# Kernel tuning notes

Hardware: AMD Instinct MI355X
Metric: run time of the kernel (lower is better)

Reference implementation:

```python
import jax, jax.numpy as jnp
import numpy as np
from jax import lax

H = 12  # num_heads (from init_kwargs)


def _orthogonal_landmarks(q, num_landmarks):
    # q: (B, N, D) already scaled. Faithful to torch loop: recursively pick the
    # point whose max |cos sim| to the already-selected landmarks is minimal.
    B, N, D = q.shape
    nrm = jnp.linalg.norm(q, axis=-1, keepdims=True)
    qk = q / jnp.maximum(nrm, 1e-12)
    bidx = jnp.arange(B)
    key = jax.random.key(42)
    idx0 = jax.random.randint(key, (B,), 0, N)
    cur = qk[bidx, idx0]                             # (B, D)
    # running max |cos sim|; selected rows pinned to 10 (as in torch code)
    max_sim = jnp.zeros((B, N), qk.dtype).at[bidx, idx0].set(10.0)

    def step(carry, _):
        max_sim, cur = carry
        cos = jnp.abs(jnp.einsum('bnd,bd->bn', qk, cur))
        max_sim = jnp.maximum(max_sim, cos)
        idx = jnp.argmin(max_sim, axis=-1)
        cur2 = qk[bidx, idx]
        max_sim = max_sim.at[bidx, idx].set(10.0)
        return (max_sim, cur2), idx

    (_, _), idxs = lax.scan(step, (max_sim, cur), None, length=num_landmarks - 1)
    all_idx = jnp.concatenate([idx0[None, :], idxs], axis=0).T  # (B, L)
    landmarks = q[bidx[:, None], all_idx]                        # unnormalized q rows
    return lax.stop_gradient(landmarks)


def _orthoformer(q, k, v, num_landmarks, num_frames):
    # q,k,v: (B*h, N, D);  N = F * P
    Bh, N, D = q.shape
    F = num_frames
    P = N // F
    sc = D ** (-0.25)
    q = q * sc
    k = k * sc
    lm = _orthogonal_landmarks(q, num_landmarks)                 # (Bh, L, D)
    kernel_1 = jax.nn.softmax(jnp.einsum('bnd,bld->bnl', q, lm), axis=-1)   # (Bh,N,L)
    k2 = jnp.einsum('bld,bnd->bln', lm, k).reshape(Bh, num_landmarks, F, P)
    kernel_2 = jax.nn.softmax(k2, axis=-1)                       # (Bh,L,F,P)
    vr = v.reshape(Bh, F, P, D)
    x = jnp.einsum('blfp,bfpd->blfd', kernel_2, vr)
    x = jnp.einsum('bnl,blfd->bnfd', kernel_1, x)                # (Bh,N,F,D)
    return x


def setup_inputs() -> dict:
    key = jax.random.key(0)
    ks = jax.random.split(key, 6)
    B, F, P, C = 2, 16, 196, 768
    N = F * P
    s = 0.02
    x = jax.random.normal(ks[0], (B, N, C), jnp.float32)
    W_qkv = jax.random.normal(ks[1], (C, 3 * C), jnp.float32) * s
    W_pq = jax.random.normal(ks[2], (C, C), jnp.float32) * s
    W_pkv = jax.random.normal(ks[3], (C, 2 * C), jnp.float32) * s
    W_proj = jax.random.normal(ks[4], (C, C), jnp.float32) * s
    b_proj = jnp.zeros((C,), jnp.float32)
    return {"x": x, "W_qkv": W_qkv, "W_pq": W_pq, "W_pkv": W_pkv,
            "W_proj": W_proj, "b_proj": b_proj,
            "seq_len": P, "num_frames": F, "num_landmarks": 128}


def reference(x, W_qkv, W_pq, W_pkv, W_proj, b_proj, seq_len, num_frames, num_landmarks):
    B, N, C = x.shape
    F, P, h = num_frames, seq_len, H
    d = C // h
    scale = d ** (-0.5)
    qkv = x @ W_qkv                                              # (B,N,3C)
    q, k, v = jnp.split(qkv, 3, axis=-1)
    def to_bh(t):  # b n (h d) -> (b h) n d
        return t.reshape(B, N, h, d).transpose(0, 2, 1, 3).reshape(B * h, N, d)
    q_, k_, v_ = to_bh(q), to_bh(k), to_bh(v)
    xo = _orthoformer(q_, k_, v_, num_landmarks, F)              # (B*h,N,F,d)
    # (b h) s f d -> b s f (h d)
    xo = xo.reshape(B, h, N, F, d).transpose(0, 2, 3, 1, 4).reshape(B, N, F, C)
    # diagonal over (frame-of-query g, frame-of-key f)
    xd = xo.reshape(B, F, P, F, C)
    xdiag = jnp.diagonal(xd, axis1=1, axis2=3)                   # (B,P,C,F)
    xdiag = jnp.moveaxis(xdiag, -1, 1).reshape(B, N, C)          # b (f p) d
    q2 = xdiag @ W_pq                                            # (B,N,C)
    k2, v2 = jnp.split(xo @ W_pkv, 2, axis=-1)                   # (B,N,F,C) each
    q2 = q2.reshape(B, N, h, d).transpose(0, 2, 1, 3) * scale    # (B,h,N,d)
    k2 = k2.reshape(B, N, F, h, d).transpose(0, 3, 1, 2, 4)      # (B,h,N,F,d)
    v2 = v2.reshape(B, N, F, h, d).transpose(0, 3, 1, 2, 4)
    attn = jax.nn.softmax(jnp.einsum('bhsd,bhsfd->bhsf', q2, k2), axis=-1)
    out = jnp.einsum('bhsf,bhsfd->bhsd', attn, v2)               # (B,h,N,d)
    out = out.transpose(0, 2, 1, 3).reshape(B, N, C)
    out = out @ W_proj + b_proj
    return out, attn
```

## Files before the change

kernel.cpp:

```cpp
#include <hip/hip_runtime.h>


using u16 = unsigned short;
using u32 = unsigned int;
using u64 = unsigned long long;

typedef short bf16x8 __attribute__((ext_vector_type(8)));
typedef float f32x4 __attribute__((ext_vector_type(4)));

#define N_ 3136
#define C_ 768
#define H_ 12
#define F_ 16
#define P_ 196
#define L_ 128
#define SC_ 0.35355339059327373f
#define OUTPART_ ((size_t)2 * N_ * C_)
#define KB_ 8
#define RPB_ 392

__device__ __forceinline__ float b2f(u16 u) {
  u32 x = ((u32)u) << 16; float f; __builtin_memcpy(&f, &x, 4); return f;
}
__device__ __forceinline__ float lo16f(u32 u) {
  u32 x = u << 16; float f; __builtin_memcpy(&f, &x, 4); return f;
}
__device__ __forceinline__ float hi16f(u32 u) {
  u32 x = u & 0xFFFF0000u; float f; __builtin_memcpy(&f, &x, 4); return f;
}
__device__ __forceinline__ u16 f2b(float f) {
  u32 u; __builtin_memcpy(&u, &f, 4);
  u32 r = (u + 0x7FFFu + ((u >> 16) & 1u)) >> 16;
  return (u16)r;
}
__device__ __forceinline__ u64 d2u(double d) { u64 u; __builtin_memcpy(&u, &d, 8); return u; }

__global__ void detect_k(const u32* __restrict__ w, int* __restrict__ flag) {
  const int t = threadIdx.x;
  int hits = 0;
  #pragma unroll
  for (int i = 0; i < 16; ++i) {
    u32 word = w[t * 16 + i];
    u32 e = (word >> 7) & 0xFFu;
    if (e >= 110u && e <= 126u) hits++;
  }
  #pragma unroll
  for (int off = 32; off > 0; off >>= 1) hits += __shfl_down(hits, off);
  if (t == 0) flag[0] = (hits >= 512) ? 0 : 1;
}

__global__ void zcnt_k(u64* __restrict__ p) { if (threadIdx.x < 384) p[threadIdx.x] = 0ull; }

__device__ __forceinline__ void tf2(u32 k0, u32 k1v, u32 c0, u32 c1, u32& o0, u32& o1) {
  u32 ks[3] = {k0, k1v, k0 ^ k1v ^ 0x1BD11BDAu};
  u32 x0 = c0 + ks[0], x1 = c1 + ks[1];
  const u32 rA[4] = {13u, 15u, 26u, 6u}, rB[4] = {17u, 29u, 16u, 24u};
  #pragma unroll
  for (int r = 0; r < 5; ++r) {
    #pragma unroll
    for (int q = 0; q < 4; ++q) {
      u32 rot = (r & 1) ? rB[q] : rA[q];
      x0 += x1; x1 = (x1 << rot) | (x1 >> (32u - rot)); x1 ^= x0;
    }
    x0 += ks[(r + 1) % 3];
    x1 += ks[(r + 2) % 3] + (u32)(r + 1);
  }
  o0 = x0; o1 = x1;
}

__device__ __forceinline__ int tf_idx0(int bh) {
  u32 a0, a1, b0, b1;
  tf2(0u, 42u, 0u, 0u, a0, a1);
  tf2(0u, 42u, 0u, 1u, b0, b1);
  u32 j = (u32)bh;
  u32 h0, h1, l0, l1;
  tf2(a0, a1, 0u, j, h0, h1);
  u32 hi = h0 ^ h1;
  tf2(b0, b1, 0u, j, l0, l1);
  u32 lo = l0 ^ l1;
  return (int)(((hi % 3136u) * 2048u + (lo % 3136u)) % 3136u);
}

__global__ __launch_bounds__(256) void qselT_k(const void* __restrict__ xr, const void* __restrict__ wr,
                                               const int* __restrict__ flagp, float* __restrict__ qt)
{
  __shared__ float As[64 * 20];
  __shared__ float Bs[16 * 64];
  const int t = threadIdx.x;
  const int m0 = blockIdx.x * 64;
  const int n0 = blockIdx.y * 64;
  const int f32i = flagp[0];
  const int tx = t & 15, ty = t >> 4;
  float acc[4][4];
  #pragma unroll
  for (int i = 0; i < 4; ++i)
    #pragma unroll
    for (int j = 0; j < 4; ++j) acc[i][j] = 0.f;

  const int alr = t >> 2;
  const int alk = (t & 3) * 4;
  const int bkr = t >> 4;
  const int bnc = (t & 15) * 4;

  for (int k0 = 0; k0 < 768; k0 += 16) {
    float4 av, bv;
    if (f32i) {
      av = *(const float4*)((const float*)xr + (size_t)(m0 + alr) * 768 + k0 + alk);
      bv = *(const float4*)((const float*)wr + (size_t)(k0 + bkr) * 2304 + n0 + bnc);
    } else {
      const u16* xa = (const u16*)xr + (size_t)(m0 + alr) * 768 + k0 + alk;
      const u16* wa = (const u16*)wr + (size_t)(k0 + bkr) * 2304 + n0 + bnc;
      av.x = b2f(xa[0]); av.y = b2f(xa[1]); av.z = b2f(xa[2]); av.w = b2f(xa[3]);
      bv.x = b2f(wa[0]); bv.y = b2f(wa[1]); bv.z = b2f(wa[2]); bv.w = b2f(wa[3]);
    }
    As[alr * 20 + alk + 0] = av.x; As[alr * 20 + alk + 1] = av.y;
    As[alr * 20 + alk + 2] = av.z; As[alr * 20 + alk + 3] = av.w;
    *(float4*)(&Bs[bkr * 64 + bnc]) = bv;
    __syncthreads();
    #pragma unroll
    for (int kk = 0; kk < 16; ++kk) {
      float a[4], b[4];
      #pragma unroll
      for (int i = 0; i < 4; ++i) a[i] = As[(ty * 4 + i) * 20 + kk];
      #pragma unroll
      for (int j = 0; j < 4; ++j) b[j] = Bs[kk * 64 + tx * 4 + j];
      #pragma unroll
      for (int i = 0; i < 4; ++i)
        #pragma unroll
        for (int j = 0; j < 4; ++j) acc[i][j] += a[i] * b[j];
    }
    __syncthreads();
  }
  #pragma unroll
  for (int i = 0; i < 4; ++i) {
    const int m = m0 + ty * 4 + i;
    const int b = m / N_, n = m - b * N_;
    #pragma unroll
    for (int j = 0; j < 4; ++j) {
      const int col = n0 + tx * 4 + j;
      const int hh = col >> 6, dd = col & 63;
      qt[((size_t)(b * H_ + hh) * 64 + dd) * N_ + n] = acc[i][j] * SC_;
    }
  }
}

__global__ __launch_bounds__(512, 1) void landmarksR_k(
    const float* __restrict__ qt, float* __restrict__ lm, u64* __restrict__ cand)
{
  const int kb = blockIdx.x;
  const int bh = blockIdx.y;
  const float* QT = qt + (size_t)bh * 64 * N_;
  float* LM = lm + (size_t)bh * L_ * 64;
  u64* cd = cand + (size_t)bh * 16;
  __shared__ double curD[64];
  __shared__ u64 redV[8];
  __shared__ int redI[8];
  __shared__ int sW;
  const int t = threadIdx.x;
  const bool act = (t < RPB_);
  const int g = t >> 2, dc = t & 3, d0 = dc * 16;
  const int r0 = kb * RPB_;
  const int myRow = r0 + t;
  const float* base = QT + r0 + 4 * g;

  float4 qreg[16];
  #pragma unroll
  for (int i = 0; i < 16; ++i) qreg[i] = (float4){0.f, 0.f, 0.f, 0.f};
  if (act) {
    #pragma unroll
    for (int i = 0; i < 16; ++i) qreg[i] = *(const float4*)(base + (size_t)(d0 + i) * N_);
  }

  double inv_own = 0.0, ms_own = 0.0;
  if (act) {
    double s0 = 0.0, s1 = 0.0, s2 = 0.0, s3 = 0.0;
    #pragma unroll
    for (int i = 0; i < 16; ++i) {
      const float4 v = qreg[i];
      s0 += (double)v.x * (double)v.x; s1 += (double)v.y * (double)v.y;
      s2 += (double)v.z * (double)v.z; s3 += (double)v.w * (double)v.w;
    }
    s0 += __shfl_xor(s0, 1); s1 += __shfl_xor(s1, 1);
    s2 += __shfl_xor(s2, 1); s3 += __shfl_xor(s3, 1);
    s0 += __shfl_xor(s0, 2); s1 += __shfl_xor(s1, 2);
    s2 += __shfl_xor(s2, 2); s3 += __shfl_xor(s3, 2);
    const double sown = (dc == 0) ? s0 : (dc == 1) ? s1 : (dc == 2) ? s2 : s3;
    inv_own = 1.0 / fmax(sqrt(sown), 1e-12);
  }
  const int idx0 = tf_idx0(bh);
  if (act && myRow == idx0) ms_own = 10.0;

  if (t < 64) {
    const float vf = QT[(size_t)t * N_ + idx0];
    double v = (double)vf;
    double s = v * v;
    #pragma unroll
    for (int off = 32; off; off >>= 1) s += __shfl_xor(s, off);
    curD[t] = v / fmax(sqrt(s), 1e-12);
    if (kb == 0) LM[t] = vf;
  }
  __syncthreads();

  for (int step = 1; step < 128; ++step) {
    u64 bV = d2u(1e30); int bI = 0x7fffffff;
    if (act) {
      double a0 = 0.0, a1 = 0.0, a2 = 0.0, a3 = 0.0;
      #pragma unroll
      for (int i = 0; i < 16; ++i) {
        const float4 v = qreg[i];
        const double c = curD[d0 + i];
        a0 += (double)v.x * c; a1 += (double)v.y * c;
        a2 += (double)v.z * c; a3 += (double)v.w * c;
      }
      a0 += __shfl_xor(a0, 1); a1 += __shfl_xor(a1, 1);
      a2 += __shfl_xor(a2, 1); a3 += __shfl_xor(a3, 1);
      a0 += __shfl_xor(a0, 2); a1 += __shfl_xor(a1, 2);
      a2 += __shfl_xor(a2, 2); a3 += __shfl_xor(a3, 2);
      const double aown = (dc == 0) ? a0 : (dc == 1) ? a1 : (dc == 2) ? a2 : a3;
      ms_own = fmax(ms_own, fabs(aown * inv_own));
      bV = d2u(ms_own); bI = myRow;
    }
    #pragma unroll
    for (int off = 32; off; off >>= 1) {
      const u64 ov = __shfl_xor(bV, off);
      const int oi = __shfl_xor(bI, off);
      if (ov < bV || (ov == bV && oi < bI)) { bV = ov; bI = oi; }
    }
    if ((t & 63) == 0) { redV[t >> 6] = bV; redI[t >> 6] = bI; }
    __syncthreads();
    const int par = step & 1;
    if (t == 0) {
      u64 v = redV[0]; int ix = redI[0];
      #pragma unroll
      for (int w2 = 1; w2 < 8; ++w2)
        if (redV[w2] < v || (redV[w2] == v && redI[w2] < ix)) { v = redV[w2]; ix = redI[w2]; }
      const u64 pk = (v & ~((1ull << 19) - 1ull)) | ((u64)(u32)(step & 127) << 12) | (u64)(u32)ix;
      __hip_atomic_store(&cd[par * KB_ + kb], pk, __ATOMIC_RELAXED, __HIP_MEMORY_SCOPE_AGENT);
    }
    if (t < 64) {
      u64 pv = ~0ull;
      int ok = 1;
      for (;;) {
        if (t < KB_) {
          pv = __hip_atomic_load(&cd[par * KB_ + t], __ATOMIC_RELAXED, __HIP_MEMORY_SCOPE_AGENT);
          ok = ((int)((pv >> 12) & 127u) == step) ? 1 : 0;
        }
        if (__all(ok)) break;
        __builtin_amdgcn_s_sleep(1);
      }
      u64 m = (t < KB_) ? pv : ~0ull;
      #pragma unroll
      for (int off = 1; off < KB_; off <<= 1) {
        const u64 o = __shfl_xor(m, off);
        if (o < m) m = o;
      }
      if (t == 0) sW = (int)(m & 0xFFFu);
    }
    __syncthreads();
    const int w = sW;
    if (act && myRow == w) ms_own = 10.0;
    if (t < 64) {
      const float vf = QT[(size_t)t * N_ + w];
      double v = (double)vf;
      double s = v * v;
      #pragma unroll
      for (int off = 32; off; off >>= 1) s += __shfl_xor(s, off);
      curD[t] = v / fmax(sqrt(s), 1e-12);
      if (kb == 0) LM[(size_t)step * 64 + t] = vf;
    }
    __syncthreads();
  }
}

__global__ __launch_bounds__(256) void twT_k(const void* __restrict__ W, int K, int Nn,
                                             const int* __restrict__ flagp, u16* __restrict__ WT)
{
  __shared__ u16 Ts[64][80];
  const int t = threadIdx.x;
  const int k0 = blockIdx.x * 64, n0 = blockIdx.y * 64;
  const int f32i = flagp[0];
  const int kr = t >> 2, nc = (t & 3) * 16;
  u16 tmp[16];
  if (f32i) {
    const float* p = (const float*)W + (size_t)(k0 + kr) * Nn + n0 + nc;
    #pragma unroll
    for (int j = 0; j < 16; ++j) tmp[j] = f2b(p[j]);
  } else {
    const u16* p = (const u16*)W + (size_t)(k0 + kr) * Nn + n0 + nc;
    #pragma unroll
    for (int j = 0; j < 16; ++j) tmp[j] = p[j];
  }
  #pragma unroll
  for (int j = 0; j < 16; ++j) Ts[kr][nc + j] = tmp[j];
  __syncthreads();
  const int nr = t >> 2, kc = (t & 3) * 16;
  u16 o[16];
  #pragma unroll
  for (int j = 0; j < 16; ++j) o[j] = Ts[kc + j][nr];
  u16* dst = WT + (size_t)(n0 + nr) * K + k0 + kc;
  *(uint4*)(dst) = *(uint4*)(o);
  *(uint4*)(dst + 8) = *(uint4*)(o + 8);
}

__global__ __launch_bounds__(256) void xcvt_k(const void* __restrict__ x,
                                              const int* __restrict__ flagp, u16* __restrict__ xb)
{
  const int i = blockIdx.x * 256 + threadIdx.x;
  if (flagp[0]) {
    const float4* p = (const float4*)x + (size_t)i * 2;
    float4 f0 = p[0], f1 = p[1];
    u16 tmp[8] = { f2b(f0.x), f2b(f0.y), f2b(f0.z), f2b(f0.w),
                   f2b(f1.x), f2b(f1.y), f2b(f1.z), f2b(f1.w) };
    *(uint4*)(xb + (size_t)i * 8) = *(uint4*)tmp;
  } else {
    ((uint4*)xb)[i] = ((const uint4*)x)[i];
  }
}

template <int MODE>
__global__ __launch_bounds__(256) void gemm_k(
    const void* __restrict__ Ap, const void* __restrict__ Bp,
    int M, int K, int lda, int ldb, int n0c, int cn, const int* __restrict__ flagp,
    float* __restrict__ of0, u16* __restrict__ ob0, u16* __restrict__ ob1, u16* __restrict__ ob2,
    const void* __restrict__ biasRaw, void* __restrict__ outRaw)
{
  __shared__ u16 As[128 * 40];
  __shared__ u16 Bs[128 * 40];
  const int t = threadIdx.x;
  const int m0 = blockIdx.x * 128;
  const int n0 = blockIdx.y * 128;
  const int rf = (MODE == 4) ? flagp[0] : 0;

  size_t aOff = 0, bOff = 0;
  if constexpr (MODE == 1) {
    const int bh = blockIdx.z;
    aOff = (size_t)bh * ((size_t)N_ * 128) + (size_t)n0c * 128;
    bOff = (size_t)bh * (1024 * 128);
  }
  const int lane = t & 63;
  const int w = t >> 6;
  const int mw = (w >> 1) * 64;
  const int nw = (w & 1) * 64;
  const int lr = lane & 15;
  const int lk = lane >> 4;

  f32x4 acc[4][4];
  #pragma unroll
  for (int i = 0; i < 4; ++i)
    #pragma unroll
    for (int j = 0; j < 4; ++j) acc[i][j] = (f32x4){0.f, 0.f, 0.f, 0.f};

  const int ar = t >> 1;
  const int ak = (t & 1) * 16;
  const int agrow = m0 + ar;
  const bool aValid = (agrow < M);
  const u16* A16 = (const u16*)Ap;
  const u16* B16 = (const u16*)Bp;

  for (int k0 = 0; k0 < K; k0 += 32) {
    uint4 a0, a1;
    if (aValid) {
      const uint4* ap = (const uint4*)(A16 + aOff + (size_t)agrow * lda + k0 + ak);
      a0 = ap[0]; a1 = ap[1];
    } else {
      a0.x = a0.y = a0.z = a0.w = 0u; a1 = a0;
    }
    const uint4* bp = (const uint4*)(B16 + bOff + (size_t)(n0 + ar) * ldb + k0 + ak);
    uint4 b0 = bp[0], b1 = bp[1];

    *(uint4*)(&As[ar * 40 + ak]) = a0;
    *(uint4*)(&As[ar * 40 + ak + 8]) = a1;
    *(uint4*)(&Bs[ar * 40 + ak]) = b0;
    *(uint4*)(&Bs[ar * 40 + ak + 8]) = b1;
    __syncthreads();

    bf16x8 af[4], bfv[4];
    #pragma unroll
    for (int mt = 0; mt < 4; ++mt)
      af[mt] = *(const bf16x8*)(&As[(mw + mt * 16 + lr) * 40 + lk * 8]);
    #pragma unroll
    for (int nt = 0; nt < 4; ++nt)
      bfv[nt] = *(const bf16x8*)(&Bs[(nw + nt * 16 + lr) * 40 + lk * 8]);
    #pragma unroll
    for (int mt = 0; mt < 4; ++mt)
      #pragma unroll
      for (int nt = 0; nt < 4; ++nt)
        acc[mt][nt] = __builtin_amdgcn_mfma_f32_16x16x32_bf16(af[mt], bfv[nt], acc[mt][nt], 0, 0, 0);
    __syncthreads();
  }

  #pragma unroll
  for (int mt = 0; mt < 4; ++mt) {
    #pragma unroll
    for (int nt = 0; nt < 4; ++nt) {
      #pragma unroll
      for (int r = 0; r < 4; ++r) {
        const int grow = m0 + mw + mt * 16 + lk * 4 + r;
        const int gcol = n0 + nw + nt * 16 + lr;
        if (grow >= M) continue;
        float vv = acc[mt][nt][r];
        if constexpr (MODE == 0) {
          int b = (grow >= N_) ? 1 : 0;
          int n = grow - b * N_;
          int t3 = gcol / C_, cc = gcol - t3 * C_;
          int hh = cc >> 6, dd = cc & 63;
          size_t dst = (((size_t)(b * H_ + hh)) * N_ + n) * 64 + dd;
          if (t3 == 0) ob0[dst] = f2b(vv * SC_);
          else if (t3 == 1) ob1[dst] = f2b(vv * SC_);
          else ob2[dst] = f2b(vv);
        } else if constexpr (MODE == 1) {
          const int bh = blockIdx.z;
          int b = bh / H_, hh = bh - b * H_;
          int f = gcol >> 6, dd = gcol & 63;
          u16 wv = f2b(vv);
          ob0[(((size_t)(b * cn + grow)) * F_ + f) * C_ + hh * 64 + dd] = wv;
          int n = n0c + grow;
          if (f == n / P_) ob1[((size_t)(b * cn + grow)) * C_ + hh * 64 + dd] = wv;
        } else if constexpr (MODE == 2) {
          const int cn16 = cn * F_;
          int b = (grow >= cn16) ? 1 : 0;
          int r2 = grow - b * cn16;
          int ln = r2 >> 4, f = r2 & 15;
          int t2 = (gcol >= C_) ? 1 : 0, cc = gcol - t2 * C_;
          int hh = cc >> 6, dd = cc & 63;
          size_t dst = ((((size_t)(b * H_ + hh)) * cn + ln) * F_ + f) * 64 + dd;
          if (t2) ob1[dst] = f2b(vv); else ob0[dst] = f2b(vv);
        } else if constexpr (MODE == 3) {
          int b = (grow >= cn) ? 1 : 0;
          int ln = grow - b * cn;
          int hh = gcol >> 6, dd = gcol & 63;
          of0[(((size_t)(b * H_ + hh)) * cn + ln) * 64 + dd] = vv * 0.125f;
        } else {
          float bvad = rf ? ((const float*)biasRaw)[gcol] : b2f(((const u16*)biasRaw)[gcol]);
          float ov = vv + bvad;
          if (rf) ((float*)outRaw)[(size_t)grow * C_ + gcol] = ov;
          else    ((u16*)outRaw)[(size_t)grow * C_ + gcol] = f2b(ov);
        }
      }
    }
  }
}

__global__ __launch_bounds__(256) void k1_k(const u16* __restrict__ qb,
                                            const float* __restrict__ lm,
                                            u16* __restrict__ k1)
{
  const int bh = blockIdx.y;
  const int r0 = blockIdx.x * 64;
  __shared__ float qT[64][65];
  __shared__ float lmS[128 * 64];
  __shared__ float redA[4][64];
  __shared__ float redB[64];
  const int t = threadIdx.x;
  const u16* Q = qb + ((size_t)bh * N_ + r0) * 64;
  const float* Lm = lm + (size_t)bh * L_ * 64;
  for (int u = t; u < 2048; u += 256) ((float4*)lmS)[u] = ((const float4*)Lm)[u];
  for (int u = t; u < 512; u += 256) {
    int row = u >> 3, j0 = (u & 7) * 8;
    uint4 pk = *(const uint4*)(Q + (size_t)row * 64 + j0);
    const u16* pu = (const u16*)&pk;
    #pragma unroll
    for (int jj = 0; jj < 8; ++jj) qT[j0 + jj][row] = b2f(pu[jj]);
  }
  __syncthreads();
  const int row = t & 63, ch = t >> 6;
  float qr[64];
  #pragma unroll
  for (int j = 0; j < 64; ++j) qr[j] = qT[j][row];
  float s[32];
  for (int li = 0; li < 32; ++li) {
    const float* lp = lmS + (ch * 32 + li) * 64;
    float a = 0.f;
    #pragma unroll
    for (int j = 0; j < 64; ++j) a += lp[j] * qr[j];
    s[li] = a;
  }
  float mx = -1e30f;
  for (int li = 0; li < 32; ++li) mx = fmaxf(mx, s[li]);
  redA[ch][row] = mx;
  __syncthreads();
  if (t < 64) redB[t] = fmaxf(fmaxf(redA[0][t], redA[1][t]), fmaxf(redA[2][t], redA[3][t]));
  __syncthreads();
  mx = redB[row];
  float sum = 0.f;
  for (int li = 0; li < 32; ++li) { float e = __expf(s[li] - mx); s[li] = e; sum += e; }
  __syncthreads();
  redA[ch][row] = sum;
  __syncthreads();
  if (t < 64) redB[t] = 1.0f / (redA[0][t] + redA[1][t] + redA[2][t] + redA[3][t]);
  __syncthreads();
  const float inv = redB[row];
  u16* out = k1 + ((size_t)bh * N_ + r0 + row) * 128 + ch * 32;
  for (int li = 0; li < 32; ++li) out[li] = f2b(s[li] * inv);
}

__global__ __launch_bounds__(256) void k2x1_k(const float* __restrict__ lm,
                                              const u16* __restrict__ kb,
                                              const u16* __restrict__ vb,
                                              u16* __restrict__ x1)
{
  const int bh = blockIdx.x;
  const int f = blockIdx.y;
  __shared__ u16 kS[P_ * 64];
  __shared__ u16 vS[P_ * 64];
  __shared__ float redM[2][128];
  __shared__ float redS[2][128];
  const int t = threadIdx.x;
  const u16* Kf = kb + ((size_t)bh * N_ + f * P_) * 64;
  const u16* Vf = vb + ((size_t)bh * N_ + f * P_) * 64;
  for (int u = t; u < 1568; u += 256) {
    ((uint4*)kS)[u] = ((const uint4*)Kf)[u];
    ((uint4*)vS)[u] = ((const uint4*)Vf)[u];
  }
  __syncthreads();
  const int l = t & 127, half = t >> 7;
  const float* lp = lm + ((size_t)bh * L_ + l) * 64;
  float lr[64];
  #pragma unroll
  for (int j = 0; j < 64; ++j) lr[j] = lp[j];

  const int p0 = half * 98, p1 = p0 + 98;
  float mx = -1e30f;
  for (int p = p0; p < p1; ++p) {
    const uint4* kp = (const uint4*)(kS + p * 64);
    float s = 0.f;
    #pragma unroll
    for (int q4 = 0; q4 < 8; ++q4) {
      uint4 pk = kp[q4];
      const u32* pu = (const u32*)&pk;
      #pragma unroll
      for (int j2 = 0; j2 < 4; ++j2) {
        u32 u = pu[j2];
        s += lr[q4 * 8 + j2 * 2] * lo16f(u) + lr[q4 * 8 + j2 * 2 + 1] * hi16f(u);
      }
    }
    mx = fmaxf(mx, s);
  }
  redM[half][l] = mx;
  __syncthreads();
  mx = fmaxf(redM[0][l], redM[1][l]);

  float sm = 0.f;
  for (int p = p0; p < p1; ++p) {
    const uint4* kp = (const uint4*)(kS + p * 64);
    float s = 0.f;
    #pragma unroll
    for (int q4 = 0; q4 < 8; ++q4) {
      uint4 pk = kp[q4];
      const u32* pu = (const u32*)&pk;
      #pragma unroll
      for (int j2 = 0; j2 < 4; ++j2) {
        u32 u = pu[j2];
        s += lr[q4 * 8 + j2 * 2] * lo16f(u) + lr[q4 * 8 + j2 * 2 + 1] * hi16f(u);
      }
    }
    sm += __expf(s - mx);
  }
  redS[half][l] = sm;
  __syncthreads();
  const float inv = 1.0f / (redS[0][l] + redS[1][l]);

  const int dd0 = half * 32;
  float acc[32];
  #pragma unroll
  for (int u = 0; u < 32; ++u) acc[u] = 0.f;
  for (int p = 0; p < P_; ++p) {
    const uint4* kp = (const uint4*)(kS + p * 64);
    float s = 0.f;
    #pragma unroll
    for (int q4 = 0; q4 < 8; ++q4) {
      uint4 pk = kp[q4];
      const u32* pu = (const u32*)&pk;
      #pragma unroll
      for (int j2 = 0; j2 < 4; ++j2) {
        u32 u = pu[j2];
        s += lr[q4 * 8 + j2 * 2] * lo16f(u) + lr[q4 * 8 + j2 * 2 + 1] * hi16f(u);
      }
    }
    const float e = __expf(s - mx);
    const uint4* vp = (const uint4*)(vS + p * 64 + dd0);
    #pragma unroll
    for (int q4 = 0; q4 < 4; ++q4) {
      uint4 pv = vp[q4];
      const u32* pu = (const u32*)&pv;
      #pragma unroll
      for (int j2 = 0; j2 < 4; ++j2) {
        u32 u = pu[j2];
        acc[q4 * 8 + j2 * 2]     += e * lo16f(u);
        acc[q4 * 8 + j2 * 2 + 1] += e * hi16f(u);
      }
    }
  }
  u16* outT = x1 + (size_t)bh * (1024 * 128) + (size_t)(f * 64 + dd0) * 128 + l;
  for (int u = 0; u < 32; ++u) outT[(size_t)u * 128] = f2b(acc[u] * inv);
}

__global__ __launch_bounds__(256) void attn_k(const float* __restrict__ q2c,
                                              const u16* __restrict__ k2c,
                                              const u16* __restrict__ v2c,
                                              int n0c, int cn, const int* __restrict__ flagp,
                                              void* __restrict__ outRaw,
                                              u16* __restrict__ o)
{
  const int bh = blockIdx.y;
  const int b = bh / H_, hh = bh - b * H_;
  const int t = threadIdx.x;
  const int f32o = flagp[0];
  __shared__ float aS[64][17];
  const int nl = t >> 2, qi = t & 3;
  const int ln = blockIdx.x * 64 + nl;
  const bool act = ln < cn;
  const int n = n0c + ln;
  float q[64];
  if (act) {
    const float* qr = q2c + ((size_t)bh * cn + ln) * 64;
    #pragma unroll
    for (int j = 0; j < 64; ++j) q[j] = qr[j];
    float lg[4];
    #pragma unroll
    for (int ff = 0; ff < 4; ++ff) {
      const int f = qi * 4 + ff;
      const u16* kp = k2c + (((size_t)bh * cn + ln) * F_ + f) * 64;
      float s = 0.f;
      #pragma unroll
      for (int j8 = 0; j8 < 8; ++j8) {
        uint4 pk = ((const uint4*)kp)[j8];
        const u16* pu = (const u16*)&pk;
        #pragma unroll
        for (int u = 0; u < 8; ++u) s += q[j8 * 8 + u] * b2f(pu[u]);
      }
      lg[ff] = s;
    }
    float mx = fmaxf(fmaxf(lg[0], lg[1]), fmaxf(lg[2], lg[3]));
    mx = fmaxf(mx, __shfl_xor(mx, 1));
    mx = fmaxf(mx, __shfl_xor(mx, 2));
    float e[4], sm = 0.f;
    #pragma unroll
    for (int ff = 0; ff < 4; ++ff) { e[ff] = __expf(lg[ff] - mx); sm += e[ff]; }
    sm += __shfl_xor(sm, 1);
    sm += __shfl_xor(sm, 2);
    const float iv = 1.0f / sm;
    const size_t abase = ((size_t)bh * N_ + n) * F_ + qi * 4;
    #pragma unroll
    for (int ff = 0; ff < 4; ++ff) {
      const float a = e[ff] * iv;
      if (f32o) ((float*)outRaw)[OUTPART_ + abase + ff] = a;
      else      ((u16*)outRaw)[OUTPART_ + abase + ff] = f2b(a);
      aS[nl][qi * 4 + ff] = a;
    }
  }
  __syncthreads();
  if (act) {
    const int dd0 = qi * 16;
    float acc[16];
    #pragma unroll
    for (int u = 0; u < 16; ++u) acc[u] = 0.f;
    for (int f = 0; f < F_; ++f) {
      const float w2 = aS[nl][f];
      const u16* vp = v2c + (((size_t)bh * cn + ln) * F_ + f) * 64 + dd0;
      uint4 pv0 = ((const uint4*)vp)[0], pv1 = ((const uint4*)vp)[1];
      const u16* pu0 = (const u16*)&pv0;
      const u16* pu1 = (const u16*)&pv1;
      #pragma unroll
      for (int u = 0; u < 8; ++u) acc[u] += w2 * b2f(pu0[u]);
      #pragma unroll
      for (int u = 0; u < 8; ++u) acc[8 + u] += w2 * b2f(pu1[u]);
    }
    u16* op = o + ((size_t)(b * N_ + n)) * C_ + hh * 64 + dd0;
    for (int u = 0; u < 16; ++u) op[u] = f2b(acc[u]);
  }
}

extern "C" void kernel_launch(void* const* d_in, const int* in_sizes, int n_in,
                              void* d_out, int out_size, void* d_ws, size_t ws_size,
                              hipStream_t stream)
{
  (void)in_sizes; (void)n_in; (void)out_size;
  const void* x     = d_in[0];
  const void* Wqkv  = d_in[1];
  const void* Wpq   = d_in[2];
  const void* Wpkv  = d_in[3];
  const void* Wproj = d_in[4];
  const void* bproj = d_in[5];

  char* ws = (char*)d_ws;
  size_t off = 0;
  auto alloc = [&](size_t bytes) { void* p = ws + off; off += (bytes + 255) & ~(size_t)255; return p; };
  int*  flagp = (int*)alloc(256);
  u16*  qb  = (u16*)alloc(9633792);
  u16*  kb  = (u16*)alloc(9633792);
  u16*  vb  = (u16*)alloc(9633792);
  float* lm = (float*)alloc(786432);
  u16*  x1b = (u16*)alloc(6291456);
  u16*  ob  = (u16*)alloc(9633792);
  const size_t k1off = off;
  u16*  k1b = (u16*)alloc(19267584);
  const size_t chunk0 = off;

  const size_t qtNeed = k1off + 19267584 + 256;

  int Nc = 0;
  {
    const int cands[5] = {3136, 1568, 784, 392, 196};
    for (int i = 0; i < 5; ++i) {
      size_t need = chunk0 + (size_t)156672 * cands[i] + 1024;
      if (need <= ws_size && qtNeed <= ws_size) { Nc = cands[i]; break; }
    }
  }
  if (Nc == 0) return;
  const int nchunks = N_ / Nc;
  u16*  xoc = (u16*)(ws + chunk0);
  u16*  k2c = xoc + (size_t)24576 * Nc;
  u16*  v2c = k2c + (size_t)24576 * Nc;
  u16*  xdc = v2c + (size_t)24576 * Nc;
  float* q2c = (float*)(xdc + (size_t)1536 * Nc);
  float* qt  = (float*)(ws + k1off);

  u16* WqkvT = (u16*)(ws + k1off);
  u16* xb    = (u16*)(ws + k1off + 3538944);
  u16* WpkvT = kb;
  u16* WpqT  = kb + 1179648;
  u16* WprojT= kb + 1179648 + 589824;

  u64* cand = (u64*)(ws + chunk0);

  detect_k<<<1, 64, 0, stream>>>((const u32*)Wqkv, flagp);
  zcnt_k<<<1, 512, 0, stream>>>(cand);

  qselT_k<<<dim3(98, 12), 256, 0, stream>>>(x, Wqkv, flagp, qt);
  landmarksR_k<<<dim3(KB_, 24), 512, 0, stream>>>(qt, lm, cand);

  twT_k<<<dim3(12, 36), 256, 0, stream>>>(Wqkv, 768, 2304, flagp, WqkvT);
  xcvt_k<<<2352, 256, 0, stream>>>(x, flagp, xb);

  gemm_k<0><<<dim3(49, 18, 1), 256, 0, stream>>>(xb, WqkvT, 6272, 768, 768, 768, 0, 0, flagp,
                                                 nullptr, qb, kb, vb, nullptr, nullptr);
  k2x1_k<<<dim3(24, 16), 256, 0, stream>>>(lm, kb, vb, x1b);
  k1_k<<<dim3(49, 24), 256, 0, stream>>>(qb, lm, k1b);

  twT_k<<<dim3(12, 24), 256, 0, stream>>>(Wpkv, 768, 1536, flagp, WpkvT);
  twT_k<<<dim3(12, 12), 256, 0, stream>>>(Wpq, 768, 768, flagp, WpqT);
  twT_k<<<dim3(12, 12), 256, 0, stream>>>(Wproj, 768, 768, flagp, WprojT);

  for (int c = 0; c < nchunks; ++c) {
    const int n0c = c * Nc;
    gemm_k<1><<<dim3((Nc + 127) / 128, 8, 24), 256, 0, stream>>>(
        k1b, x1b, Nc, 128, 128, 128, n0c, Nc, flagp, nullptr, xoc, xdc, nullptr, nullptr, nullptr);
    gemm_k<2><<<dim3((2 * Nc * 16) / 128, 12, 1), 256, 0, stream>>>(
        xoc, WpkvT, 2 * Nc * 16, 768, 768, 768, n0c, Nc, flagp, nullptr, k2c, v2c, nullptr, nullptr, nullptr);
    gemm_k<3><<<dim3((2 * Nc + 127) / 128, 6, 1), 256, 0, stream>>>(
        xdc, WpqT, 2 * Nc, 768, 768, 768, n0c, Nc, flagp, q2c, nullptr, nullptr, nullptr, nullptr, nullptr);
    attn_k<<<dim3((Nc + 63) / 64, 24), 256, 0, stream>>>(
        q2c, k2c, v2c, n0c, Nc, flagp, d_out, ob);
  }
  gemm_k<4><<<dim3(49, 6, 1), 256, 0, stream>>>(ob, WprojT, 6272, 768, 768, 768, 0, 0, flagp,
                                                nullptr, nullptr, nullptr, nullptr, bproj, d_out);
}
```

Before: 1.782 ms.

## Load GEMM tiles directly to LDS with global_load_lds and XOR swizzle

Replaces the register-staged global-to-shared copies in the templated GEMM with direct global_load_lds 16-byte transfers into LDS. The padded 40-stride layout becomes an unpadded 32-stride layout with an XOR swizzle on the 8-element segment index, so MFMA fragment reads stay conflict-free. Out-of-range A rows are clamped to the last valid row instead of being zero-filled. This is meant to cut VGPR traffic and instruction count in the load path, at the cost of relying on the hardware's direct-to-LDS write ordering and on the clamped rows never reaching the output.

```diff
diff --git a/kernel.cpp b/kernel.cpp
--- a/kernel.cpp
+++ b/kernel.cpp
@@ -34,6 +34,12 @@
   return (u16)r;
 }
 __device__ __forceinline__ u64 d2u(double d) { u64 u; __builtin_memcpy(&u, &d, 8); return u; }
+
+__device__ __forceinline__ void gll16(const void* g, void* l) {
+  __builtin_amdgcn_global_load_lds(
+      (__attribute__((address_space(1))) void*)g,
+      (__attribute__((address_space(3))) void*)l, 16, 0, 0);
+}
 
 __global__ void detect_k(const u32* __restrict__ w, int* __restrict__ flag) {
   const int t = threadIdx.x;
@@ -324,8 +330,8 @@
     float* __restrict__ of0, u16* __restrict__ ob0, u16* __restrict__ ob1, u16* __restrict__ ob2,
     const void* __restrict__ biasRaw, void* __restrict__ outRaw)
 {
-  __shared__ u16 As[128 * 40];
-  __shared__ u16 Bs[128 * 40];
+  __shared__ u16 As[128 * 32];
+  __shared__ u16 Bs[128 * 32];
   const int t = threadIdx.x;
   const int m0 = blockIdx.x * 128;
   const int n0 = blockIdx.y * 128;
@@ -350,37 +356,43 @@
     #pragma unroll
     for (int j = 0; j < 4; ++j) acc[i][j] = (f32x4){0.f, 0.f, 0.f, 0.f};
 
-  const int ar = t >> 1;
-  const int ak = (t & 1) * 16;
-  const int agrow = m0 + ar;
-  const bool aValid = (agrow < M);
+  const int c0 = w * 2, c1 = c0 + 1;
+  const int rl = lane >> 2, sl = lane & 3;
+  const int rowA0 = c0 * 16 + rl, rowA1 = c1 * 16 + rl;
+  const int segA0 = (sl ^ ((rowA0 ^ (rowA0 >> 2)) & 3)) * 8;
+  const int segA1 = (sl ^ ((rowA1 ^ (rowA1 >> 2)) & 3)) * 8;
+  int ga0 = m0 + rowA0; if (ga0 >= M) ga0 = M - 1;
+  int ga1 = m0 + rowA1; if (ga1 >= M) ga1 = M - 1;
   const u16* A16 = (const u16*)Ap;
   const u16* B16 = (const u16*)Bp;
+  const u16* aP0 = A16 + aOff + (size_t)ga0 * lda + segA0;
+  const u16* aP1 = A16 + aOff + (size_t)ga1 * lda + segA1;
+  const u16* bP0 = B16 + bOff + (size_t)(n0 + rowA0) * ldb + segA0;
+  const u16* bP1 = B16 + bOff + (size_t)(n0 + rowA1) * ldb + segA1;
+  u16* lA0 = &As[c0 * 512]; u16* lA1 = &As[c1 * 512];
+  u16* lB0 = &Bs[c0 * 512]; u16* lB1 = &Bs[c1 * 512];
+
+  int roA[4], roB[4];
+  #pragma unroll
+  for (int q = 0; q < 4; ++q) {
+    const int ra = mw + q * 16 + lr;
+    roA[q] = ra * 32 + ((lk ^ ((ra ^ (ra >> 2)) & 3)) * 8);
+    const int rb = nw + q * 16 + lr;
+    roB[q] = rb * 32 + ((lk ^ ((rb ^ (rb >> 2)) & 3)) * 8);
+  }
 
   for (int k0 = 0; k0 < K; k0 += 32) {
-    uint4 a0, a1;
-    if (aValid) {
-      const uint4* ap = (const uint4*)(A16 + aOff + (size_t)agrow * lda + k0 + ak);
-      a0 = ap[0]; a1 = ap[1];
-    } else {
-      a0.x = a0.y = a0.z = a0.w = 0u; a1 = a0;
-    }
-    const uint4* bp = (const uint4*)(B16 + bOff + (size_t)(n0 + ar) * ldb + k0 + ak);
-    uint4 b0 = bp[0], b1 = bp[1];
-
-    *(uint4*)(&As[ar * 40 + ak]) = a0;
-    *(uint4*)(&As[ar * 40 + ak + 8]) = a1;
-    *(uint4*)(&Bs[ar * 40 + ak]) = b0;
-    *(uint4*)(&Bs[ar * 40 + ak + 8]) = b1;
+    gll16(aP0 + k0, lA0);
+    gll16(aP1 + k0, lA1);
+    gll16(bP0 + k0, lB0);
+    gll16(bP1 + k0, lB1);
     __syncthreads();
 
     bf16x8 af[4], bfv[4];
     #pragma unroll
-    for (int mt = 0; mt < 4; ++mt)
-      af[mt] = *(const bf16x8*)(&As[(mw + mt * 16 + lr) * 40 + lk * 8]);
-    #pragma unroll
-    for (int nt = 0; nt < 4; ++nt)
-      bfv[nt] = *(const bf16x8*)(&Bs[(nw + nt * 16 + lr) * 40 + lk * 8]);
+    for (int mt = 0; mt < 4; ++mt) af[mt] = *(const bf16x8*)(&As[roA[mt]]);
+    #pragma unroll
+    for (int nt = 0; nt < 4; ++nt) bfv[nt] = *(const bf16x8*)(&Bs[roB[nt]]);
     #pragma unroll
     for (int mt = 0; mt < 4; ++mt)
       #pragma unroll
```

After: 1.770 ms. Within noise of the previous version (-0.7%).
